# Performance work log

Hardware: AMD Instinct MI355X
Metric: run time of the kernel (lower is better)

## Reference

```python
import jax, jax.numpy as jnp
import numpy as np

NUM_USERS = 200000
NUM_ITEMS = 100000
DIM = 64
NUM_LAYERS = 2
NUM_EDGES = 3200000
EPS = 1e-12  # F.normalize eps


def setup_inputs() -> dict:
    key = jax.random.key(0)
    ks = jax.random.split(key, 8)
    return {
        "user_emb": jax.random.normal(ks[0], (NUM_USERS, DIM), dtype=jnp.float32),
        "item_emb": jax.random.normal(ks[1], (NUM_ITEMS, DIM), dtype=jnp.float32),
        "Wu": jax.random.normal(ks[2], (NUM_LAYERS, DIM, 2 * DIM), dtype=jnp.float32) * 0.1,
        "Wi": jax.random.normal(ks[3], (NUM_LAYERS, DIM, 2 * DIM), dtype=jnp.float32) * 0.1,
        "u_idx": jax.random.randint(ks[4], (NUM_EDGES,), 0, NUM_USERS, dtype=jnp.int32),
        "i_idx": jax.random.randint(ks[5], (NUM_EDGES,), 0, NUM_ITEMS, dtype=jnp.int32),
        "w_u2i": jax.random.uniform(ks[6], (NUM_EDGES,), dtype=jnp.float32),
        "w_i2u": jax.random.uniform(ks[7], (NUM_EDGES,), dtype=jnp.float32),
    }


def _l2_normalize(x):
    # matches F.normalize(p=2, dim=1): x / max(||x||, eps)
    n = jnp.sqrt(jnp.sum(x * x, axis=1, keepdims=True))
    return x / jnp.maximum(n, EPS)


def _spmm(vals, rows, cols, h, num_rows):
    # (sparse [num_rows, num_cols]) @ h : gather rows of h at cols, scale, scatter-add
    msg = vals[:, None] * h[cols]  # [E, DIM]
    return jax.ops.segment_sum(msg, rows, num_segments=num_rows)


def reference(user_emb, item_emb, Wu, Wi, u_idx, i_idx, w_u2i, w_i2u):
    h_u, h_i = user_emb, item_emb
    for l in range(NUM_LAYERS):
        neigh_u = _spmm(w_u2i, u_idx, i_idx, h_i, NUM_USERS)   # adj_u2i @ h_i
        neigh_i = _spmm(w_i2u, i_idx, u_idx, h_u, NUM_ITEMS)   # adj_i2u @ h_u
        # Linear(2*dim -> dim, no bias): concat then x @ W.T
        h_u_new = jax.nn.relu(jnp.concatenate([h_u, neigh_u], axis=1) @ Wu[l].T)
        h_i_new = jax.nn.relu(jnp.concatenate([h_i, neigh_i], axis=1) @ Wi[l].T)
        h_u = _l2_normalize(h_u_new)
        h_i = _l2_normalize(h_i_new)
    return (h_u, h_i)
```

## Files before the change

### kernel.cpp

```cpp
#include <hip/hip_runtime.h>


#define N_USERS 200000
#define N_ITEMS 100000
#define N_EDGES 3200000
#define NB_U 782
#define NB_I 391

__global__ __launch_bounds__(256) void wprep_kernel(
    const float* __restrict__ Wu, const float* __restrict__ Wi,
    float* __restrict__ WuT, float* __restrict__ WiT)
{
    int idx = blockIdx.x * 256 + threadIdx.x;
    const float* src = Wu;
    float* dst = WuT;
    int i = idx;
    if (idx >= 16384) { src = Wi; dst = WiT; i = idx - 16384; }
    int l = i >> 13;
    int r = i & 8191;
    int j = r >> 7;
    int k = r & 127;
    dst[l * 8192 + k * 64 + j] = src[i];
}

__global__ __launch_bounds__(256) void hist_kernel(
    const int* __restrict__ u_idx, const int* __restrict__ i_idx,
    int* __restrict__ deg_u, int* __restrict__ deg_i,
    unsigned short* __restrict__ rank_u, unsigned short* __restrict__ rank_i)
{
    int t = blockIdx.x * 256 + threadIdx.x;
    if (t < N_EDGES) {
        rank_u[t] = (unsigned short)atomicAdd(&deg_u[u_idx[t]], 1);
    } else {
        int e = t - N_EDGES;
        rank_i[e] = (unsigned short)atomicAdd(&deg_i[i_idx[e]], 1);
    }
}

__global__ __launch_bounds__(256) void scanA_kernel(
    const int* __restrict__ deg_u, const int* __restrict__ deg_i,
    int* __restrict__ bsum_u, int* __restrict__ bsum_i)
{
    int b = blockIdx.x;
    const int* deg; int n; int* bs; int bb;
    if (b < NB_U) { deg = deg_u; n = N_USERS; bs = bsum_u; bb = b; }
    else          { deg = deg_i; n = N_ITEMS; bs = bsum_i; bb = b - NB_U; }
    int i = bb * 256 + threadIdx.x;
    int v = (i < n) ? deg[i] : 0;
    #pragma unroll
    for (int off = 1; off < 64; off <<= 1) v += __shfl_xor(v, off);
    __shared__ int ws4[4];
    int wv = threadIdx.x >> 6;
    if ((threadIdx.x & 63) == 0) ws4[wv] = v;
    __syncthreads();
    if (threadIdx.x == 0) bs[bb] = ws4[0] + ws4[1] + ws4[2] + ws4[3];
}

__global__ __launch_bounds__(1024) void scanB_kernel(
    const int* __restrict__ bsum_u, int* __restrict__ bpre_u,
    const int* __restrict__ bsum_i, int* __restrict__ bpre_i)
{
    __shared__ int s[1024];
    const int* src; int* dst; int n;
    if (blockIdx.x == 0) { src = bsum_u; dst = bpre_u; n = NB_U; }
    else                 { src = bsum_i; dst = bpre_i; n = NB_I; }
    int t = threadIdx.x;
    int v = (t < n) ? src[t] : 0;
    s[t] = v; __syncthreads();
    #pragma unroll
    for (int off = 1; off < 1024; off <<= 1) {
        int x = (t >= off) ? s[t - off] : 0;
        __syncthreads();
        s[t] += x;
        __syncthreads();
    }
    if (t < n) dst[t] = s[t] - v;
}

__global__ __launch_bounds__(256) void scanC_kernel(
    const int* __restrict__ deg_u, const int* __restrict__ deg_i,
    const int* __restrict__ bpre_u, const int* __restrict__ bpre_i,
    int* __restrict__ rowptr_u, int* __restrict__ rowptr_i)
{
    int b = blockIdx.x;
    const int* deg; int n; const int* bpre; int* rowptr; int bb;
    if (b < NB_U) { deg = deg_u; n = N_USERS; bpre = bpre_u; rowptr = rowptr_u; bb = b; }
    else          { deg = deg_i; n = N_ITEMS; bpre = bpre_i; rowptr = rowptr_i; bb = b - NB_U; }
    int t = threadIdx.x;
    int i = bb * 256 + t;
    int d = (i < n) ? deg[i] : 0;
    __shared__ int s[256];
    s[t] = d; __syncthreads();
    #pragma unroll
    for (int off = 1; off < 256; off <<= 1) {
        int x = (t >= off) ? s[t - off] : 0;
        __syncthreads();
        s[t] += x;
        __syncthreads();
    }
    int val = bpre[bb] + (s[t] - d);
    if (i < n) rowptr[i] = val;
    if (b == 0 && t == 0) { rowptr_u[N_USERS] = N_EDGES; rowptr_i[N_ITEMS] = N_EDGES; }
}

__global__ __launch_bounds__(256) void fill_kernel(
    const int* __restrict__ u_idx, const int* __restrict__ i_idx,
    const float* __restrict__ w_u2i, const float* __restrict__ w_i2u,
    const unsigned short* __restrict__ rank_u, const unsigned short* __restrict__ rank_i,
    const int* __restrict__ rowptr_u, const int* __restrict__ rowptr_i,
    uint2* __restrict__ edges_u, uint2* __restrict__ edges_i)
{
    const int part   = blockIdx.x & 7;
    const int slot   = blockIdx.x >> 3;
    const int nslots = gridDim.x >> 3;
    const int stride = nslots * 256;

    for (int e = slot * 256 + threadIdx.x; e < N_EDGES; e += stride) {
        int ru = u_idx[e];
        int ri = i_idx[e];
        if ((ru & 7) == part) {
            int p = rowptr_u[ru] + rank_u[e];
            edges_u[p] = make_uint2((unsigned)ri, __float_as_uint(w_u2i[e]));
        }
        if ((ri & 7) == part) {
            int p = rowptr_i[ri] + rank_i[e];
            edges_i[p] = make_uint2((unsigned)ru, __float_as_uint(w_i2u[e]));
        }
    }
}

__global__ __launch_bounds__(256, 4) void transform_fused_kernel(
    const float* __restrict__ hself_u, const float* __restrict__ hsrc_u,
    const int* __restrict__ rowptr_u, const uint2* __restrict__ edges_u,
    const float* __restrict__ WtU, float* __restrict__ out_u,
    const float* __restrict__ hself_i, const float* __restrict__ hsrc_i,
    const int* __restrict__ rowptr_i, const uint2* __restrict__ edges_i,
    const float* __restrict__ WtI, float* __restrict__ out_i,
    int nbu)
{
    __shared__ float Ws[64 * 64];
    __shared__ float Xs[64 * 68];
    __shared__ int   rp_s[65];

    const int tid = threadIdx.x;

    const float* hself; const float* hsrc; const int* rowptr;
    const uint2* edges; const float* Wt; float* out; int N; int bb;
    if ((int)blockIdx.x < nbu) {
        hself = hself_u; hsrc = hsrc_u; rowptr = rowptr_u; edges = edges_u;
        Wt = WtU; out = out_u; N = N_USERS; bb = blockIdx.x;
    } else {
        hself = hself_i; hsrc = hsrc_i; rowptr = rowptr_i; edges = edges_i;
        Wt = WtI; out = out_i; N = N_ITEMS; bb = blockIdx.x - nbu;
    }
    const int row0 = bb * 64;

    #pragma unroll
    for (int i = 0; i < 16; ++i) Ws[tid + i * 256] = Wt[tid + i * 256];
    #pragma unroll
    for (int i = 0; i < 16; ++i) {
        int idx = tid + i * 256;
        int rr = idx >> 6, cc = idx & 63;
        int gr = row0 + rr; if (gr > N - 1) gr = N - 1;
        Xs[rr * 68 + cc] = hself[gr * 64 + cc];
    }
    if (tid <= 64) rp_s[tid] = rowptr[min(row0 + tid, N)];
    __syncthreads();

    const int tr = tid >> 3;
    const int tc = tid & 7;
    const int r0 = 2 * tr;

    float acc[2][8];
    #pragma unroll
    for (int j = 0; j < 2; ++j)
        #pragma unroll
        for (int c = 0; c < 8; ++c) acc[j][c] = 0.f;

    #pragma unroll 8
    for (int k = 0; k < 64; ++k) {
        float a0 = Xs[r0 * 68 + k];
        float a1 = Xs[(r0 + 1) * 68 + k];
        float4 b0 = *(const float4*)&Ws[k * 64 + 8 * tc];
        float4 b1 = *(const float4*)&Ws[k * 64 + 8 * tc + 4];
        float b[8] = {b0.x, b0.y, b0.z, b0.w, b1.x, b1.y, b1.z, b1.w};
        #pragma unroll
        for (int c = 0; c < 8; ++c) {
            acc[0][c] = fmaf(a0, b[c], acc[0][c]);
            acc[1][c] = fmaf(a1, b[c], acc[1][c]);
        }
    }
    __syncthreads();

    {
        const float4* src = (const float4*)(Wt + 4096);
        float4* dst = (float4*)Ws;
        #pragma unroll
        for (int i = 0; i < 4; ++i) dst[tid + i * 256] = src[tid + i * 256];
        #pragma unroll
        for (int i = 0; i < 17; ++i) Xs[tid + i * 256] = 0.f;
    }
    __syncthreads();

    {
        const int wv = tid >> 6;
        const int ln = tid & 63;
        const int e0 = rp_s[0], e1 = rp_s[64];
        const int perw = (e1 - e0 + 3) >> 2;
        const int wsb  = e0 + wv * perw;
        const int web  = min(wsb + perw, e1);
        const int clen = (web - wsb + 7) >> 3;

        int   cs[8], ce[8], rr[8], nend[8];
        float gacc[8];
        uint2 ec[8];
        #pragma unroll
        for (int c = 0; c < 8; ++c) {
            cs[c] = wsb + c * clen;
            ce[c] = min(cs[c] + clen, web);
            gacc[c] = 0.f;
            int lo = 0, hi = 64;
            #pragma unroll
            for (int s = 0; s < 6; ++s) {
                int mid = (lo + hi) >> 1;
                bool go = rp_s[mid] <= cs[c];
                lo = go ? mid : lo;
                hi = go ? hi : mid;
            }
            rr[c] = lo; nend[c] = rp_s[lo + 1];
            ec[c] = edges[min(cs[c], N_EDGES - 1)];
        }

        #pragma unroll 1
        for (int it = 0; it < clen; ++it) {
            float hv[8], wg[8];
            #pragma unroll
            for (int c = 0; c < 8; ++c) {
                bool v = (cs[c] + it) < ce[c];
                wg[c] = v ? __uint_as_float(ec[c].y) : 0.f;
                hv[c] = hsrc[(int)ec[c].x * 64 + ln];
            }
            #pragma unroll
            for (int c = 0; c < 8; ++c)
                ec[c] = edges[min(cs[c] + it + 1, N_EDGES - 1)];
            #pragma unroll
            for (int c = 0; c < 8; ++c) {
                gacc[c] = fmaf(wg[c], hv[c], gacc[c]);
                int p   = cs[c] + it;
                int nxt = p + 1;
                if (p < ce[c] && (nxt == nend[c] || nxt == ce[c])) {
                    atomicAdd(&Xs[rr[c] * 68 + ln], gacc[c]);
                    gacc[c] = 0.f;
                    if (nxt == nend[c] && nxt < web) {
                        int r2 = rr[c];
                        while (r2 < 63 && rp_s[r2 + 1] <= nxt) ++r2;
                        rr[c] = r2; nend[c] = rp_s[r2 + 1];
                    }
                }
            }
        }
    }
    __syncthreads();

    #pragma unroll 8
    for (int k = 0; k < 64; ++k) {
        float a0 = Xs[r0 * 68 + k];
        float a1 = Xs[(r0 + 1) * 68 + k];
        float4 b0 = *(const float4*)&Ws[k * 64 + 8 * tc];
        float4 b1 = *(const float4*)&Ws[k * 64 + 8 * tc + 4];
        float b[8] = {b0.x, b0.y, b0.z, b0.w, b1.x, b1.y, b1.z, b1.w};
        #pragma unroll
        for (int c = 0; c < 8; ++c) {
            acc[0][c] = fmaf(a0, b[c], acc[0][c]);
            acc[1][c] = fmaf(a1, b[c], acc[1][c]);
        }
    }

    #pragma unroll
    for (int j = 0; j < 2; ++j) {
        float s = 0.f;
        #pragma unroll
        for (int c = 0; c < 8; ++c) {
            float v = fmaxf(acc[j][c], 0.f);
            acc[j][c] = v;
            s = fmaf(v, v, s);
        }
        s += __shfl_xor(s, 1);
        s += __shfl_xor(s, 2);
        s += __shfl_xor(s, 4);
        float nrm = sqrtf(s);
        float inv = 1.f / fmaxf(nrm, 1e-12f);
        int gr = row0 + r0 + j;
        if (gr < N) {
            float4 o0 = make_float4(acc[j][0]*inv, acc[j][1]*inv, acc[j][2]*inv, acc[j][3]*inv);
            float4 o1 = make_float4(acc[j][4]*inv, acc[j][5]*inv, acc[j][6]*inv, acc[j][7]*inv);
            float* p = out + gr * 64 + 8 * tc;
            *(float4*)p       = o0;
            *(float4*)(p + 4) = o1;
        }
    }
}

extern "C" void kernel_launch(void* const* d_in, const int* in_sizes, int n_in,
                              void* d_out, int out_size, void* d_ws, size_t ws_size,
                              hipStream_t stream)
{
    (void)in_sizes; (void)n_in; (void)out_size; (void)ws_size;

    const float* user_emb = (const float*)d_in[0];
    const float* item_emb = (const float*)d_in[1];
    const float* Wu       = (const float*)d_in[2];
    const float* Wi       = (const float*)d_in[3];
    const int*   u_idx    = (const int*)d_in[4];
    const int*   i_idx    = (const int*)d_in[5];
    const float* w_u2i    = (const float*)d_in[6];
    const float* w_i2u    = (const float*)d_in[7];
    float* out = (float*)d_out;

    float* ws      = (float*)d_ws;
    float* WuT     = ws;
    float* WiT     = WuT + 16384;
    float* hu1     = WiT + 16384;
    float* hi1     = hu1 + N_USERS * 64;
    uint2* edges_u = (uint2*)(hi1 + N_ITEMS * 64);
    uint2* edges_i = edges_u + N_EDGES;
    unsigned short* rank_u = (unsigned short*)(edges_i + N_EDGES);
    unsigned short* rank_i = rank_u + N_EDGES;
    int* rowptr_u = (int*)(rank_i + N_EDGES);
    int* rowptr_i = rowptr_u + (N_USERS + 1);
    int* deg_u    = rowptr_i + (N_ITEMS + 1);
    int* deg_i    = deg_u + N_USERS;
    int* bsum_u   = deg_i + N_ITEMS;
    int* bpre_u   = bsum_u + NB_U;
    int* bsum_i   = bpre_u + NB_U;
    int* bpre_i   = bsum_i + NB_I;

    const int tu_blocks = (N_USERS + 63) / 64;
    const int ti_blocks = (N_ITEMS + 63) / 64;
    const int e2_blocks = (2 * N_EDGES) / 256;

    wprep_kernel<<<128, 256, 0, stream>>>(Wu, Wi, WuT, WiT);
    hipMemsetAsync(deg_u, 0, (size_t)(N_USERS + N_ITEMS) * 4, stream);
    hist_kernel<<<e2_blocks, 256, 0, stream>>>(u_idx, i_idx, deg_u, deg_i, rank_u, rank_i);
    scanA_kernel<<<NB_U + NB_I, 256, 0, stream>>>(deg_u, deg_i, bsum_u, bsum_i);
    scanB_kernel<<<2, 1024, 0, stream>>>(bsum_u, bpre_u, bsum_i, bpre_i);
    scanC_kernel<<<NB_U + NB_I, 256, 0, stream>>>(deg_u, deg_i, bpre_u, bpre_i, rowptr_u, rowptr_i);
    fill_kernel<<<2048, 256, 0, stream>>>(u_idx, i_idx, w_u2i, w_i2u,
                                          rank_u, rank_i, rowptr_u, rowptr_i,
                                          edges_u, edges_i);

    transform_fused_kernel<<<tu_blocks + ti_blocks, 256, 0, stream>>>(
        user_emb, item_emb, rowptr_u, edges_u, WuT, hu1,
        item_emb, user_emb, rowptr_i, edges_i, WiT, hi1, tu_blocks);

    transform_fused_kernel<<<tu_blocks + ti_blocks, 256, 0, stream>>>(
        hu1, hi1, rowptr_u, edges_u, WuT + 8192, out,
        hi1, hu1, rowptr_i, edges_i, WiT + 8192, out + (size_t)N_USERS * 64, tu_blocks);
}
```

Measured before the change: 1.348 ms.

## Pack local row id into edge records and atomically accumulate per edge

Each CSR edge record now carries the destination row's low 6 bits, packed above an 18-bit source index. The gather loop reads the local row straight from the record instead of binary-searching rowptr and tracking row boundaries per chunk. Chunk splitting becomes exact integer partitioning with a single guarded tail step, and the edge arrays are padded by 8 entries so the prefetch can over-read safely. The trade-off is one LDS atomicAdd per edge instead of one per row segment, which raises LDS atomic traffic in exchange for less branching and simpler control flow.

```diff
diff --git a/kernel.cpp b/kernel.cpp
--- a/kernel.cpp
+++ b/kernel.cpp
@@ -120,11 +120,13 @@
         int ri = i_idx[e];
         if ((ru & 7) == part) {
             int p = rowptr_u[ru] + rank_u[e];
-            edges_u[p] = make_uint2((unsigned)ri, __float_as_uint(w_u2i[e]));
+            edges_u[p] = make_uint2((unsigned)ri | ((unsigned)(ru & 63) << 18),
+                                    __float_as_uint(w_u2i[e]));
         }
         if ((ri & 7) == part) {
             int p = rowptr_i[ri] + rank_i[e];
-            edges_i[p] = make_uint2((unsigned)ru, __float_as_uint(w_i2u[e]));
+            edges_i[p] = make_uint2((unsigned)ru | ((unsigned)(ri & 63) << 18),
+                                    __float_as_uint(w_i2u[e]));
         }
     }
 }
@@ -205,58 +207,50 @@
     {
         const int wv = tid >> 6;
         const int ln = tid & 63;
-        const int e0 = rp_s[0], e1 = rp_s[64];
-        const int perw = (e1 - e0 + 3) >> 2;
-        const int wsb  = e0 + wv * perw;
-        const int web  = min(wsb + perw, e1);
-        const int clen = (web - wsb + 7) >> 3;
-
-        int   cs[8], ce[8], rr[8], nend[8];
-        float gacc[8];
+        const int e0 = rp_s[0];
+        const int E  = rp_s[64] - e0;
+        const int wbeg = e0 + ((wv * E) >> 2);
+        const int wend = e0 + (((wv + 1) * E) >> 2);
+        const int L = wend - wbeg;
+
+        int   pos[8], ce[8];
         uint2 ec[8];
         #pragma unroll
         for (int c = 0; c < 8; ++c) {
-            cs[c] = wsb + c * clen;
-            ce[c] = min(cs[c] + clen, web);
-            gacc[c] = 0.f;
-            int lo = 0, hi = 64;
-            #pragma unroll
-            for (int s = 0; s < 6; ++s) {
-                int mid = (lo + hi) >> 1;
-                bool go = rp_s[mid] <= cs[c];
-                lo = go ? mid : lo;
-                hi = go ? hi : mid;
-            }
-            rr[c] = lo; nend[c] = rp_s[lo + 1];
-            ec[c] = edges[min(cs[c], N_EDGES - 1)];
-        }
+            pos[c] = wbeg + ((c * L) >> 3);
+            ce[c]  = wbeg + (((c + 1) * L) >> 3);
+            ec[c]  = edges[pos[c]];
+        }
+        const int Lf = L >> 3;
 
         #pragma unroll 1
-        for (int it = 0; it < clen; ++it) {
+        for (int it = 0; it < Lf; ++it) {
             float hv[8], wg[8];
+            int   rl[8];
             #pragma unroll
             for (int c = 0; c < 8; ++c) {
-                bool v = (cs[c] + it) < ce[c];
-                wg[c] = v ? __uint_as_float(ec[c].y) : 0.f;
-                hv[c] = hsrc[(int)ec[c].x * 64 + ln];
+                unsigned x = ec[c].x;
+                wg[c] = __uint_as_float(ec[c].y);
+                rl[c] = (int)(x >> 18);
+                hv[c] = hsrc[(int)(x & 0x3FFFFu) * 64 + ln];
+            }
+            #pragma unroll
+            for (int c = 0; c < 8; ++c) {
+                ++pos[c];
+                ec[c] = edges[pos[c]];
             }
             #pragma unroll
             for (int c = 0; c < 8; ++c)
-                ec[c] = edges[min(cs[c] + it + 1, N_EDGES - 1)];
+                atomicAdd(&Xs[rl[c] * 68 + ln], wg[c] * hv[c]);
+        }
+        {
             #pragma unroll
             for (int c = 0; c < 8; ++c) {
-                gacc[c] = fmaf(wg[c], hv[c], gacc[c]);
-                int p   = cs[c] + it;
-                int nxt = p + 1;
-                if (p < ce[c] && (nxt == nend[c] || nxt == ce[c])) {
-                    atomicAdd(&Xs[rr[c] * 68 + ln], gacc[c]);
-                    gacc[c] = 0.f;
-                    if (nxt == nend[c] && nxt < web) {
-                        int r2 = rr[c];
-                        while (r2 < 63 && rp_s[r2 + 1] <= nxt) ++r2;
-                        rr[c] = r2; nend[c] = rp_s[r2 + 1];
-                    }
-                }
+                bool v = pos[c] < ce[c];
+                unsigned x = v ? ec[c].x : 0u;
+                float  w = v ? __uint_as_float(ec[c].y) : 0.f;
+                float hv = hsrc[(int)(x & 0x3FFFFu) * 64 + ln];
+                atomicAdd(&Xs[(int)(x >> 18) * 68 + ln], w * hv);
             }
         }
     }
@@ -323,8 +317,8 @@
     float* hu1     = WiT + 16384;
     float* hi1     = hu1 + N_USERS * 64;
     uint2* edges_u = (uint2*)(hi1 + N_ITEMS * 64);
-    uint2* edges_i = edges_u + N_EDGES;
-    unsigned short* rank_u = (unsigned short*)(edges_i + N_EDGES);
+    uint2* edges_i = edges_u + (N_EDGES + 8);
+    unsigned short* rank_u = (unsigned short*)(edges_i + (N_EDGES + 8));
     unsigned short* rank_i = rank_u + N_EDGES;
     int* rowptr_u = (int*)(rank_i + N_EDGES);
     int* rowptr_i = rowptr_u + (N_USERS + 1);
```

After: 5.125 ms. 3.8x slower.
